# Kernel tuning notes

Hardware: AMD Instinct MI355X
Metric: run time of the kernel (lower is better)

## Reference

```python
import jax, jax.numpy as jnp
import numpy as np

N_NODES = 50000
N_EDGES = 800000
D = 128

def setup_inputs() -> dict:
    key = jax.random.key(0)
    k1, k2, k3, k4 = jax.random.split(key, 4)
    x = jax.random.normal(k1, (N_NODES, D), dtype=jnp.float32)
    edge_index = jax.random.randint(k2, (2, N_EDGES), 0, N_NODES, dtype=jnp.int64)
    # nn.Linear params: W is (out_dim, in_dim), b is (out_dim,)
    W = jax.random.normal(k3, (D, D), dtype=jnp.float32) * (1.0 / np.sqrt(D))
    b = jax.random.normal(k4, (D,), dtype=jnp.float32) * 0.01
    return {"x": x, "edge_index": edge_index, "W": W, "b": b}

def reference(x, edge_index, W, b):
    row, col = edge_index[0], edge_index[1]
    h = x @ W.T + b                      # (N, D) linear projection
    msgs = h[col]                        # gather by source col, (E, D)
    agg = jax.ops.segment_sum(msgs, row, num_segments=N_NODES)  # scatter-add by row
    return agg + h                       # residual
```

## Files before the change

kernel.cpp:

```cpp
#include <hip/hip_runtime.h>

#define NN 50000
#define NE 800000
#define DD 128
#define TILE_M 64
#define WPAD 136
#define CAP 64

#define NBG ((NN + TILE_M - 1) / TILE_M)
#define ECHUNK 2048
#define NCH ((NE + ECHUNK - 1) / ECHUNK)
#define NBS (NCH * 8)

typedef __attribute__((ext_vector_type(8))) short short8;
typedef __attribute__((ext_vector_type(4))) float f32x4;

__device__ __forceinline__ unsigned short f2bf(float f) {
    unsigned int u = __float_as_uint(f);
    u += 0x7fffu + ((u >> 16) & 1u);
    return (unsigned short)(u >> 16);
}

__global__ __launch_bounds__(256) void fused_gemm_scatter(
    const float* __restrict__ x, const float* __restrict__ W,
    const float* __restrict__ b, const int* __restrict__ ei,
    float* __restrict__ out, unsigned short* __restrict__ hbf,
    int* __restrict__ deg, int* __restrict__ slots)
{
    if (blockIdx.x >= NBG) {
        const int part  = blockIdx.x & 7;
        const int chunk = (blockIdx.x - NBG) >> 3;
        const int base  = chunk * ECHUNK;
#pragma unroll
        for (int i = 0; i < 8; ++i) {
            const int e = base + i * 256 + threadIdx.x;
            if (e < NE) {
                const int r = ei[e];
                if ((r & 7) == part) {
                    const int c = ei[NE + e];
                    const int p = atomicAdd(&deg[r], 1);
                    if (p < CAP) slots[r * CAP + p] = c;
                }
            }
        }
        return;
    }

    __shared__ unsigned short Wl[128 * WPAD];
    __shared__ unsigned short xl[TILE_M * WPAD];

    const int t = threadIdx.x;

    for (int i = t; i < 128 * 32; i += 256) {
        const int r = i >> 5, c4 = (i & 31) << 2;
        const float4 w4 = *(const float4*)(W + r * 128 + c4);
        unsigned short* dst = &Wl[r * WPAD + c4];
        dst[0] = f2bf(w4.x); dst[1] = f2bf(w4.y);
        dst[2] = f2bf(w4.z); dst[3] = f2bf(w4.w);
    }

    const int row0 = blockIdx.x * TILE_M;
#pragma unroll
    for (int i = 0; i < 8; ++i) {
        const int idx = i * 256 + t;
        const int r = idx >> 5, c4 = (idx & 31) << 2;
        int gr = row0 + r; if (gr > NN - 1) gr = NN - 1;
        const float4 v = *(const float4*)(x + (size_t)gr * 128 + c4);
        unsigned short* dst = &xl[r * WPAD + c4];
        dst[0] = f2bf(v.x); dst[1] = f2bf(v.y);
        dst[2] = f2bf(v.z); dst[3] = f2bf(v.w);
    }

    const int lane = t & 63;
    const int wave = t >> 6;
    const int m16  = lane & 15;
    const int quad = lane >> 4;

    float bias[8];
#pragma unroll
    for (int nt = 0; nt < 8; ++nt) bias[nt] = b[nt * 16 + m16];

    __syncthreads();

    const int am = wave * 16 + m16;
    short8 afrag[4];
#pragma unroll
    for (int kc = 0; kc < 4; ++kc)
        afrag[kc] = *(const short8*)&xl[am * WPAD + kc * 32 + quad * 8];

    f32x4 acc[8];
#pragma unroll
    for (int nt = 0; nt < 8; ++nt) acc[nt] = (f32x4){0.f, 0.f, 0.f, 0.f};

#pragma unroll
    for (int kc = 0; kc < 4; ++kc) {
#pragma unroll
        for (int nt = 0; nt < 8; ++nt) {
            const short8 bfrag =
                *(const short8*)&Wl[(nt * 16 + m16) * WPAD + kc * 32 + quad * 8];
            acc[nt] = __builtin_amdgcn_mfma_f32_16x16x32_bf16(
                afrag[kc], bfrag, acc[nt], 0, 0, 0);
        }
    }

    const int rbase = row0 + wave * 16 + quad * 4;
#pragma unroll
    for (int nt = 0; nt < 8; ++nt) {
#pragma unroll
        for (int r = 0; r < 4; ++r) {
            const int grow = rbase + r;
            if (grow < NN) {
                const float v = acc[nt][r] + bias[nt];
                out[(size_t)grow * 128 + nt * 16 + m16] = v;
                hbf[(size_t)grow * 128 + nt * 16 + m16] = f2bf(v);
            }
        }
    }
}

__global__ __launch_bounds__(256) void agg_kernel(
    const int* __restrict__ deg, const int* __restrict__ slots,
    const unsigned short* __restrict__ hbf, float* __restrict__ out)
{
    const int n = (blockIdx.x * 256 + threadIdx.x) >> 6;
    if (n >= NN) return;
    const int lane = threadIdx.x & 63;
    const int g = lane >> 4;
    const int s = lane & 15;

    const int dn_raw = deg[n];
    const int idx    = slots[n * CAP + lane];
    float4 r0, r1;
    if (g == 0) {
        r0 = *(const float4*)(out + (size_t)n * 128 + s * 8);
        r1 = *(const float4*)(out + (size_t)n * 128 + s * 8 + 4);
    }
    const int dn = min(dn_raw, CAP);

    float acc[8];
#pragma unroll
    for (int i = 0; i < 8; ++i) acc[i] = 0.f;

    for (int k = 0; k < dn; k += 16) {
        uint4 p[4];
#pragma unroll
        for (int bb = 0; bb < 4; ++bb) {
            const int e = k + bb * 4 + g;
            const int c = __shfl(idx, e, 64);
            p[bb] = (uint4){0u, 0u, 0u, 0u};
            if (e < dn)
                p[bb] = *(const uint4*)(hbf + (size_t)c * 128 + s * 8);
        }
#pragma unroll
        for (int bb = 0; bb < 4; ++bb) {
            acc[0] += __uint_as_float(p[bb].x << 16);
            acc[1] += __uint_as_float(p[bb].x & 0xffff0000u);
            acc[2] += __uint_as_float(p[bb].y << 16);
            acc[3] += __uint_as_float(p[bb].y & 0xffff0000u);
            acc[4] += __uint_as_float(p[bb].z << 16);
            acc[5] += __uint_as_float(p[bb].z & 0xffff0000u);
            acc[6] += __uint_as_float(p[bb].w << 16);
            acc[7] += __uint_as_float(p[bb].w & 0xffff0000u);
        }
    }

#pragma unroll
    for (int i = 0; i < 8; ++i) acc[i] += __shfl_xor(acc[i], 16, 64);
#pragma unroll
    for (int i = 0; i < 8; ++i) acc[i] += __shfl_xor(acc[i], 32, 64);

    if (g == 0) {
        r0.x += acc[0]; r0.y += acc[1]; r0.z += acc[2]; r0.w += acc[3];
        r1.x += acc[4]; r1.y += acc[5]; r1.z += acc[6]; r1.w += acc[7];
        *(float4*)(out + (size_t)n * 128 + s * 8)     = r0;
        *(float4*)(out + (size_t)n * 128 + s * 8 + 4) = r1;
    }
}

extern "C" void kernel_launch(void* const* d_in, const int* in_sizes, int n_in,
                              void* d_out, int out_size, void* d_ws, size_t ws_size,
                              hipStream_t stream)
{
    const float* x  = (const float*)d_in[0];
    const int*   ei = (const int*)d_in[1];
    const float* W  = (const float*)d_in[2];
    const float* b  = (const float*)d_in[3];
    float* out = (float*)d_out;

    unsigned short* hbf   = (unsigned short*)d_ws;
    int*            slots = (int*)(hbf + (size_t)NN * DD);
    int*            deg   = slots + (size_t)NN * CAP;

    hipMemsetAsync(deg, 0, NN * sizeof(int), stream);

    fused_gemm_scatter<<<NBG + NBS, 256, 0, stream>>>(x, W, b, ei, out, hbf, deg, slots);

    agg_kernel<<<(NN * 64 + 255) / 256, 256, 0, stream>>>(deg, slots, hbf, out);
}
```

Before: 163.9 us.

## Drop LDS staging in GEMM; pre-convert W to bf16 in prologue kernel

A small prologue kernel now zeroes the degree array, replacing the memset, and converts W to bf16 once into workspace. The GEMM blocks then load A fragments straight from global x and B fragments straight from global bf16 W, with no shared-memory staging and no __syncthreads. The aim is to stop every block re-converting W, cut LDS use so more blocks fit per CU (launch bounds now request 6), and remove the barrier. The cost is uncoalesced, repeated global or cache reads of W fragments by every wave, plus one extra kernel launch.

New measurement: 165.5 us. Within noise of the previous version (+1.0%).

```diff
diff --git a/kernel.cpp b/kernel.cpp
--- a/kernel.cpp
+++ b/kernel.cpp
@@ -4,7 +4,6 @@
 #define NE 800000
 #define DD 128
 #define TILE_M 64
-#define WPAD 136
 #define CAP 64
 
 #define NBG ((NN + TILE_M - 1) / TILE_M)
@@ -21,8 +20,25 @@
     return (unsigned short)(u >> 16);
 }
 
-__global__ __launch_bounds__(256) void fused_gemm_scatter(
-    const float* __restrict__ x, const float* __restrict__ W,
+__global__ __launch_bounds__(256) void prologue(
+    const float* __restrict__ W, unsigned short* __restrict__ Wbf,
+    int* __restrict__ deg)
+{
+    const int t = blockIdx.x * 256 + threadIdx.x;
+    for (int i = t; i < NN; i += 64 * 256) deg[i] = 0;
+    if (blockIdx.x == 0) {
+        for (int i = threadIdx.x; i < 128 * 32; i += 256) {
+            const float4 w4 = ((const float4*)W)[i];
+            ushort4 s4;
+            s4.x = f2bf(w4.x); s4.y = f2bf(w4.y);
+            s4.z = f2bf(w4.z); s4.w = f2bf(w4.w);
+            *(ushort4*)(Wbf + i * 4) = s4;
+        }
+    }
+}
+
+__global__ __launch_bounds__(256, 6) void fused_gemm_scatter(
+    const float* __restrict__ x, const unsigned short* __restrict__ Wbf,
     const float* __restrict__ b, const int* __restrict__ ei,
     float* __restrict__ out, unsigned short* __restrict__ hbf,
     int* __restrict__ deg, int* __restrict__ slots)
@@ -46,47 +62,28 @@
         return;
     }
 
-    __shared__ unsigned short Wl[128 * WPAD];
-    __shared__ unsigned short xl[TILE_M * WPAD];
-
-    const int t = threadIdx.x;
-
-    for (int i = t; i < 128 * 32; i += 256) {
-        const int r = i >> 5, c4 = (i & 31) << 2;
-        const float4 w4 = *(const float4*)(W + r * 128 + c4);
-        unsigned short* dst = &Wl[r * WPAD + c4];
-        dst[0] = f2bf(w4.x); dst[1] = f2bf(w4.y);
-        dst[2] = f2bf(w4.z); dst[3] = f2bf(w4.w);
-    }
-
-    const int row0 = blockIdx.x * TILE_M;
-#pragma unroll
-    for (int i = 0; i < 8; ++i) {
-        const int idx = i * 256 + t;
-        const int r = idx >> 5, c4 = (idx & 31) << 2;
-        int gr = row0 + r; if (gr > NN - 1) gr = NN - 1;
-        const float4 v = *(const float4*)(x + (size_t)gr * 128 + c4);
-        unsigned short* dst = &xl[r * WPAD + c4];
-        dst[0] = f2bf(v.x); dst[1] = f2bf(v.y);
-        dst[2] = f2bf(v.z); dst[3] = f2bf(v.w);
-    }
-
+    const int t    = threadIdx.x;
     const int lane = t & 63;
     const int wave = t >> 6;
     const int m16  = lane & 15;
     const int quad = lane >> 4;
 
-    float bias[8];
-#pragma unroll
-    for (int nt = 0; nt < 8; ++nt) bias[nt] = b[nt * 16 + m16];
+    const int row0 = blockIdx.x * TILE_M;
+    int gr = row0 + wave * 16 + m16;
+    if (gr > NN - 1) gr = NN - 1;
 
-    __syncthreads();
-
-    const int am = wave * 16 + m16;
     short8 afrag[4];
 #pragma unroll
-    for (int kc = 0; kc < 4; ++kc)
-        afrag[kc] = *(const short8*)&xl[am * WPAD + kc * 32 + quad * 8];
+    for (int kc = 0; kc < 4; ++kc) {
+        const float4 a0 = *(const float4*)(x + (size_t)gr * 128 + kc * 32 + quad * 8);
+        const float4 a1 = *(const float4*)(x + (size_t)gr * 128 + kc * 32 + quad * 8 + 4);
+        short8 af;
+        af[0] = (short)f2bf(a0.x); af[1] = (short)f2bf(a0.y);
+        af[2] = (short)f2bf(a0.z); af[3] = (short)f2bf(a0.w);
+        af[4] = (short)f2bf(a1.x); af[5] = (short)f2bf(a1.y);
+        af[6] = (short)f2bf(a1.z); af[7] = (short)f2bf(a1.w);
+        afrag[kc] = af;
+    }
 
     f32x4 acc[8];
 #pragma unroll
@@ -97,7 +94,7 @@
 #pragma unroll
         for (int nt = 0; nt < 8; ++nt) {
             const short8 bfrag =
-                *(const short8*)&Wl[(nt * 16 + m16) * WPAD + kc * 32 + quad * 8];
+                *(const short8*)(Wbf + (nt * 16 + m16) * 128 + kc * 32 + quad * 8);
             acc[nt] = __builtin_amdgcn_mfma_f32_16x16x32_bf16(
                 afrag[kc], bfrag, acc[nt], 0, 0, 0);
         }
@@ -106,11 +103,12 @@
     const int rbase = row0 + wave * 16 + quad * 4;
 #pragma unroll
     for (int nt = 0; nt < 8; ++nt) {
+        const float bias = b[nt * 16 + m16];
 #pragma unroll
         for (int r = 0; r < 4; ++r) {
             const int grow = rbase + r;
             if (grow < NN) {
-                const float v = acc[nt][r] + bias[nt];
+                const float v = acc[nt][r] + bias;
                 out[(size_t)grow * 128 + nt * 16 + m16] = v;
                 hbf[(size_t)grow * 128 + nt * 16 + m16] = f2bf(v);
             }
@@ -190,10 +188,11 @@
     unsigned short* hbf   = (unsigned short*)d_ws;
     int*            slots = (int*)(hbf + (size_t)NN * DD);
     int*            deg   = slots + (size_t)NN * CAP;
+    unsigned short* Wbf   = (unsigned short*)(deg + NN);
 
-    hipMemsetAsync(deg, 0, NN * sizeof(int), stream);
+    prologue<<<64, 256, 0, stream>>>(W, Wbf, deg);
 
-    fused_gemm_scatter<<<NBG + NBS, 256, 0, stream>>>(x, W, b, ei, out, hbf, deg, slots);
+    fused_gemm_scatter<<<NBG + NBS, 256, 0, stream>>>(x, Wbf, b, ei, out, hbf, deg, slots);
 
     agg_kernel<<<(NN * 64 + 255) / 256, 256, 0, stream>>>(deg, slots, hbf, out);
 }
```
